# Kernel tuning notes

Hardware: AMD Instinct MI355X
Metric: run time of the kernel (lower is better)

## Reference

```python
import jax, jax.numpy as jnp
import numpy as np

D, H = 8, 1024        # data_dim, hidden_size
ENC, HOR = 96, 336    # encode window, prediction horizon


def _cell(x, h, c, wih, whh, b):
    # PyTorch LSTM gate order: i, f, g, o
    g = x @ wih.T + h @ whh.T + b
    i, f, gg, o = jnp.split(g, 4, axis=-1)
    c2 = jax.nn.sigmoid(f) * c + jax.nn.sigmoid(i) * jnp.tanh(gg)
    h2 = jax.nn.sigmoid(o) * jnp.tanh(c2)
    return h2, c2


def _run_layer(xs, wih, whh, b, h0, c0):
    # xs: [T, B, in] -> outputs [T, B, out], final (h, c)
    def step(carry, xt):
        h, c = carry
        h2, c2 = _cell(xt, h, c, wih, whh, b)
        return (h2, c2), h2
    (hT, cT), hs = jax.lax.scan(step, (h0, c0), xs)
    return hs, hT, cT


def setup_inputs() -> dict:
    key = jax.random.key(0)
    ks = jax.random.split(key, 10)
    s = 1.0 / np.sqrt(H)
    inputs = jax.random.normal(ks[0], (64, ENC + HOR, D), dtype=jnp.float32)
    # lstm (2 layers, hidden H)
    w_ih0 = jax.random.normal(ks[1], (4 * H, D), dtype=jnp.float32) * s
    w_hh0 = jax.random.normal(ks[2], (4 * H, H), dtype=jnp.float32) * s
    b0 = jax.random.normal(ks[3], (4 * H,), dtype=jnp.float32) * s
    w_ih1 = jax.random.normal(ks[4], (4 * H, H), dtype=jnp.float32) * s
    w_hh1 = jax.random.normal(ks[5], (4 * H, H), dtype=jnp.float32) * s
    b1 = jax.random.normal(ks[6], (4 * H,), dtype=jnp.float32) * s
    # lstm2 (1 layer, hidden D)
    w_ih2 = jax.random.normal(ks[7], (4 * D, H), dtype=jnp.float32) * s
    w_hh2 = jax.random.normal(ks[8], (4 * D, D), dtype=jnp.float32) * s
    b2 = jax.random.normal(ks[9], (4 * D,), dtype=jnp.float32) * s
    return {"inputs": inputs, "w_ih0": w_ih0, "w_hh0": w_hh0, "b0": b0,
            "w_ih1": w_ih1, "w_hh1": w_hh1, "b1": b1,
            "w_ih2": w_ih2, "w_hh2": w_hh2, "b2": b2}


def reference(inputs, w_ih0, w_hh0, b0, w_ih1, w_hh1, b1, w_ih2, w_hh2, b2):
    x = inputs[..., :D]
    enc, y = x[:, :ENC], x[:, ENC:]          # [B,96,D], [B,336,D]
    B = enc.shape[0]
    zH = jnp.zeros((B, H), dtype=enc.dtype)
    zD = jnp.zeros((B, D), dtype=enc.dtype)

    # ---- encode: stacked LSTM over 96 steps ----
    xs = enc.transpose(1, 0, 2)              # [T,B,D]
    h1s, ha, ca = _run_layer(xs, w_ih0, w_hh0, b0, zH, zH)
    h2s, hb, cb = _run_layer(h1s, w_ih1, w_hh1, b1, zH, zH)
    hds, hd, cd = _run_layer(h2s, w_ih2, w_hh2, b2, zD, zD)
    pred0 = hds[-1]                          # [B,D]

    def dec(carry, _):
        p, ha, ca, hb, cb, hd, cd = carry
        ha, ca = _cell(p, ha, ca, w_ih0, w_hh0, b0)
        hb, cb = _cell(ha, hb, cb, w_ih1, w_hh1, b1)
        hd, cd = _cell(hb, hd, cd, w_ih2, w_hh2, b2)
        return (hd, ha, ca, hb, cb, hd, cd), hd

    _, preds = jax.lax.scan(dec, (pred0, ha, ca, hb, cb, hd, cd), None,
                            length=HOR - 1)  # [335,B,D]
    pred = jnp.concatenate([pred0[None], preds], axis=0).transpose(1, 0, 2)  # [B,336,D]
    loss = jnp.mean((pred - y) ** 2, axis=(0, 1))  # [D]
    return pred, y, loss
```

## Files before the change

### kernel.cpp

```cpp
#include <hip/hip_runtime.h>
#include <math.h>

#define B64 64
#define H 1024
#define DD 8
#define ENC 96
#define HOR 336
#define TT 432
#define NSTEP 431
#define NBLK 256
#define KS0 32
#define KS1 64

typedef __attribute__((ext_vector_type(8))) short short8;
typedef __attribute__((ext_vector_type(4))) float f32x4;
typedef unsigned long long ull;

__device__ __forceinline__ unsigned short f2bf(float x) {
    union { float f; unsigned u; } v; v.f = x;
    unsigned r = v.u + 0x7fffu + ((v.u >> 16) & 1u);
    return (unsigned short)(r >> 16);
}
__device__ __forceinline__ float sigm(float x) {
    return __builtin_amdgcn_rcpf(1.0f + __expf(-x));
}
__device__ __forceinline__ float ftanh(float x) {
    float e = __expf(fminf(x, 10.0f) * 2.0f);
    return (e - 1.0f) * __builtin_amdgcn_rcpf(e + 1.0f);
}

__device__ __forceinline__ short8 cload(const unsigned short* p) {
    const ull* q = (const ull*)p;
    ull lo = __hip_atomic_load(q,     __ATOMIC_RELAXED, __HIP_MEMORY_SCOPE_AGENT);
    ull hi = __hip_atomic_load(q + 1, __ATOMIC_RELAXED, __HIP_MEMORY_SCOPE_AGENT);
    union { ull u[2]; short8 s; } v; v.u[0] = lo; v.u[1] = hi;
    return v.s;
}
__device__ __forceinline__ void cstore8(ull* p, ull v) {
    __hip_atomic_store(p, v, __ATOMIC_RELAXED, __HIP_MEMORY_SCOPE_AGENT);
}


__global__ void zero_k(unsigned int* __restrict__ p, int n) {
    for (int i = blockIdx.x * 256 + threadIdx.x; i < n; i += gridDim.x * 256) p[i] = 0u;
}

__global__ void pack0_k(const float* __restrict__ w, unsigned short* __restrict__ dst) {
    const int total = 128 * 2 * KS0 * 64 * 8;
    for (int idx = blockIdx.x * 256 + threadIdx.x; idx < total; idx += gridDim.x * 256) {
        int j = idx & 7, lane = (idx >> 3) & 63, ks = (idx >> 9) & 31, nt = (idx >> 14) & 1, nb = idx >> 15;
        int rr = nt * 16 + (lane & 15);
        int row = nb * 8 + (rr >> 2) + 1024 * (rr & 3);
        int k = ks * 32 + ((lane >> 4) << 3) + j;
        dst[idx] = f2bf(w[row * 1024 + k]);
    }
}

__global__ void pack1_k(const float* __restrict__ wih, const float* __restrict__ whh,
                        unsigned short* __restrict__ dst) {
    const int total = 128 * 2 * KS1 * 64 * 8;
    for (int idx = blockIdx.x * 256 + threadIdx.x; idx < total; idx += gridDim.x * 256) {
        int j = idx & 7, lane = (idx >> 3) & 63, ks = (idx >> 9) & 63, nt = (idx >> 15) & 1, nb = idx >> 16;
        int rr = nt * 16 + (lane & 15);
        int row = nb * 8 + (rr >> 2) + 1024 * (rr & 3);
        int k = ks * 32 + ((lane >> 4) << 3) + j;
        float v = (k < 1024) ? wih[row * 1024 + k] : whh[row * 1024 + (k - 1024)];
        dst[idx] = f2bf(v);
    }
}

__global__ void pack2_k(const float* __restrict__ w, unsigned short* __restrict__ dst) {
    const int total = 2 * KS0 * 64 * 8;
    for (int idx = blockIdx.x * 256 + threadIdx.x; idx < total; idx += gridDim.x * 256) {
        int j = idx & 7, lane = (idx >> 3) & 63, ks = (idx >> 9) & 31, nt = (idx >> 14) & 1;
        int rr = nt * 16 + (lane & 15);
        int row = (rr >> 2) + 8 * (rr & 3);
        int k = ks * 32 + ((lane >> 4) << 3) + j;
        dst[idx] = f2bf(w[row * 1024 + k]);
    }
}

__global__ void copy_y_k(const float* __restrict__ inp, float* __restrict__ y) {
    const int total = B64 * HOR * DD;
    for (int i = blockIdx.x * 256 + threadIdx.x; i < total; i += gridDim.x * 256) {
        int b = i / (HOR * DD);
        int rem = i - b * (HOR * DD);
        y[i] = inp[b * (TT * DD) + ENC * DD + rem];
    }
}

__global__ void loss_k(const float* __restrict__ pred, const float* __restrict__ y,
                       float* __restrict__ loss) {
    __shared__ float part[256];
    int tid = threadIdx.x;
    int dd = tid & 7, cc = tid >> 3;
    float s = 0.f;
    for (int i = cc; i < B64 * HOR; i += 32) {
        float d = pred[i * 8 + dd] - y[i * 8 + dd];
        s += d * d;
    }
    part[tid] = s;
    __syncthreads();
    if (tid < 8) {
        float t = 0.f;
        for (int r = 0; r < 32; ++r) t += part[r * 8 + tid];
        loss[tid] = t / (float)(B64 * HOR);
    }
}

__device__ __forceinline__ void gbar_arrive(unsigned* dom, int rb, unsigned ep) {
    if (threadIdx.x == 0) {
        __builtin_amdgcn_s_waitcnt(0x0f70);
        __hip_atomic_store(dom + rb * 32, ep, __ATOMIC_RELAXED,
                           __HIP_MEMORY_SCOPE_SYSTEM);
    }
}
__device__ __forceinline__ void gbar_wait(unsigned* dom, unsigned ep) {
    const int tid = threadIdx.x;
    if (tid < 64) {
        const unsigned* f0 = dom + tid * 32;
        const unsigned* f1 = dom + (tid + 64) * 32;
        for (;;) {
            unsigned a = __hip_atomic_load(f0, __ATOMIC_RELAXED, __HIP_MEMORY_SCOPE_SYSTEM);
            unsigned b = __hip_atomic_load(f1, __ATOMIC_RELAXED, __HIP_MEMORY_SCOPE_SYSTEM);
            if (__all((a >= ep) && (b >= ep))) break;
        }
    }
    __syncthreads();
}

__global__ __launch_bounds__(256, 1) void persist_k(
    const unsigned short* __restrict__ Wp0,
    const unsigned short* __restrict__ Wp1,
    const unsigned short* __restrict__ Wp2,
    const float* __restrict__ wih0, const float* __restrict__ b0v,
    const float* __restrict__ b1v,
    const float* __restrict__ whh2, const float* __restrict__ b2v,
    const float* __restrict__ inp,
    unsigned short* __restrict__ H0a, unsigned short* __restrict__ H0b,
    unsigned short* __restrict__ H1a, unsigned short* __restrict__ H1b,
    unsigned* __restrict__ bar0, float* __restrict__ pred)
{
    const int tid = threadIdx.x;
    const int wv = tid >> 6, lane = tid & 63;
    const int blk = blockIdx.x;
    const int bg = blk & 1, rb = blk >> 1;
    const int bl = tid & 31, u = tid >> 5;
    const int mtl = bl >> 4, m16 = bl & 15;
    unsigned* dom = bar0 + (bg << 13);

    __shared__ float red1[16 * 272];
    __shared__ float red2[16 * 272];
    __shared__ float h2x[32 * 9];
    __shared__ ull hstage[32][2];

    for (int i = tid; i < 32 * 9; i += 256) h2x[i] = 0.f;

    short8 Wr0[2][8], Wr1h0[2][8], Wr1h1[2][8];
    {
        const short8* p0 = (const short8*)Wp0;
        const short8* p1 = (const short8*)Wp1;
        #pragma unroll
        for (int ot = 0; ot < 2; ++ot)
            #pragma unroll
            for (int kk = 0; kk < 8; ++kk) {
                Wr0[ot][kk]   = p0[((rb * 2 + ot) * KS0 + 8 * wv + kk) * 64 + lane];
                Wr1h0[ot][kk] = p1[((rb * 2 + ot) * KS1 + 8 * wv + kk) * 64 + lane];
                Wr1h1[ot][kk] = p1[((rb * 2 + ot) * KS1 + 32 + 8 * wv + kk) * 64 + lane];
            }
    }
    float wih0r[4][8], whh2r[4][8], b0r[4], b1r[4], b2r[4];
    #pragma unroll
    for (int g = 0; g < 4; ++g) {
        int row = rb * 8 + u + 1024 * g;
        #pragma unroll
        for (int d = 0; d < 8; ++d) wih0r[g][d] = wih0[row * 8 + d];
        b0r[g] = b0v[row];
        b1r[g] = b1v[row];
        int row2 = u + 8 * g;
        #pragma unroll
        for (int d = 0; d < 8; ++d) whh2r[g][d] = whh2[row2 * 8 + d];
        b2r[g] = b2v[row2];
    }
    float c0r = 0.f, c1r = 0.f, c2r = 0.f;
    unsigned ep = 0;

    auto redWrite = [&](float* red, f32x4 (&acc)[2][2]) {
        #pragma unroll
        for (int m = 0; m < 2; ++m)
            #pragma unroll
            for (int ot = 0; ot < 2; ++ot) {
                int base = ((wv * 2 + m) * 2 + ot) * 272 + (lane & 15) * 17 + (lane >> 4) * 4;
                #pragma unroll
                for (int r = 0; r < 4; ++r) red[base + r] = acc[m][ot][r];
            }
    };
    auto redSum = [&](const float* red, int g) {
        int rr = u * 4 + g, ot = rr >> 4, rr16 = rr & 15;
        float s = 0.f;
        #pragma unroll
        for (int w2 = 0; w2 < 4; ++w2)
            s += red[((w2 * 2 + mtl) * 2 + ot) * 272 + rr16 * 17 + m16];
        return s;
    };
    auto hPublish = [&](unsigned short* Hw) {
        __syncthreads();
        if (tid < 32) {
            int b = bg * 32 + tid;
            int chunk = ((b >> 4) * KS0 + (rb >> 2)) * 64 + ((b & 15) | ((rb & 3) << 4));
            cstore8((ull*)Hw + chunk * 2,     hstage[tid][0]);
            cstore8((ull*)Hw + chunk * 2 + 1, hstage[tid][1]);
        }
    };

    short8 qa[8], qb[8];
    {
        union { ull u[2]; short8 s; } z; z.u[0] = 0; z.u[1] = 0;
        #pragma unroll
        for (int kk = 0; kk < 8; ++kk) { qa[kk] = z.s; qb[kk] = z.s; }
    }
    __syncthreads();

    {
        float xv[8];
        int b = bg * 32 + bl;
        #pragma unroll
        for (int d = 0; d < 8; ++d) xv[d] = inp[(b * TT + 0) * DD + d];
        float g4[4];
        #pragma unroll
        for (int g = 0; g < 4; ++g) {
            float s = b0r[g];
            #pragma unroll
            for (int d = 0; d < 8; ++d) s += wih0r[g][d] * xv[d];
            g4[g] = s;
        }
        c0r = sigm(g4[0]) * ftanh(g4[2]);
        float hn = sigm(g4[3]) * ftanh(c0r);
        ((unsigned short*)hstage)[bl * 8 + u] = f2bf(hn);
        hPublish(H0a);
    }
    gbar_arrive(dom, rb, ++ep);

    short8 pa[8], pb[8];

    for (int t = 0; t < NSTEP; ++t) {
        const int par = t & 1;
        const unsigned short* H0cur = par ? H0b : H0a;
        unsigned short* H1w = par ? H1b : H1a;
        unsigned short* H0nxt = par ? H0a : H0b;
        const bool last = (t == NSTEP - 1);

        f32x4 acc[2][2];
        #pragma unroll
        for (int m = 0; m < 2; ++m)
            #pragma unroll
            for (int ot = 0; ot < 2; ++ot) acc[m][ot] = (f32x4){0.f, 0.f, 0.f, 0.f};
        #pragma unroll
        for (int kk = 0; kk < 8; ++kk) {
            #pragma unroll
            for (int ot = 0; ot < 2; ++ot) {
                acc[0][ot] = __builtin_amdgcn_mfma_f32_16x16x32_bf16(qa[kk], Wr1h1[ot][kk], acc[0][ot], 0, 0, 0);
                acc[1][ot] = __builtin_amdgcn_mfma_f32_16x16x32_bf16(qb[kk], Wr1h1[ot][kk], acc[1][ot], 0, 0, 0);
            }
        }
        gbar_wait(dom, ep);

        {
            #pragma unroll
            for (int kk = 0; kk < 8; ++kk) {
                pa[kk] = cload(H0cur + (((bg * 2 + 0) * KS0 + 8 * wv + kk) * 64 + lane) * 8);
                pb[kk] = cload(H0cur + (((bg * 2 + 1) * KS0 + 8 * wv + kk) * 64 + lane) * 8);
            }
            #pragma unroll
            for (int kk = 0; kk < 8; ++kk) {
                #pragma unroll
                for (int ot = 0; ot < 2; ++ot) {
                    acc[0][ot] = __builtin_amdgcn_mfma_f32_16x16x32_bf16(pa[kk], Wr1h0[ot][kk], acc[0][ot], 0, 0, 0);
                    acc[1][ot] = __builtin_amdgcn_mfma_f32_16x16x32_bf16(pb[kk], Wr1h0[ot][kk], acc[1][ot], 0, 0, 0);
                }
            }
            redWrite(red1, acc);
            __syncthreads();
            float g4[4];
            #pragma unroll
            for (int g = 0; g < 4; ++g) g4[g] = b1r[g] + redSum(red1, g);
            c1r = sigm(g4[1]) * c1r + sigm(g4[0]) * ftanh(g4[2]);
            float hn = sigm(g4[3]) * ftanh(c1r);
            ((unsigned short*)hstage)[bl * 8 + u] = f2bf(hn);
            hPublish(H1w);
        }
        gbar_arrive(dom, rb, ++ep);

        if (!last) {
            f32x4 a1[2][2];
            #pragma unroll
            for (int m = 0; m < 2; ++m)
                #pragma unroll
                for (int ot = 0; ot < 2; ++ot) a1[m][ot] = (f32x4){0.f, 0.f, 0.f, 0.f};
            #pragma unroll
            for (int kk = 0; kk < 8; ++kk) {
                #pragma unroll
                for (int ot = 0; ot < 2; ++ot) {
                    a1[0][ot] = __builtin_amdgcn_mfma_f32_16x16x32_bf16(pa[kk], Wr0[ot][kk], a1[0][ot], 0, 0, 0);
                    a1[1][ot] = __builtin_amdgcn_mfma_f32_16x16x32_bf16(pb[kk], Wr0[ot][kk], a1[1][ot], 0, 0, 0);
                }
            }
            redWrite(red2, a1);
        }
        gbar_wait(dom, ep);

        {
            const short8* p2w = (const short8*)Wp2;
            short8 w2[2][8];
            #pragma unroll
            for (int ot = 0; ot < 2; ++ot)
                #pragma unroll
                for (int kk = 0; kk < 8; ++kk)
                    w2[ot][kk] = p2w[(ot * KS0 + 8 * wv + kk) * 64 + lane];
            #pragma unroll
            for (int kk = 0; kk < 8; ++kk) {
                qa[kk] = cload(H1w + (((bg * 2 + 0) * KS0 + 8 * wv + kk) * 64 + lane) * 8);
                qb[kk] = cload(H1w + (((bg * 2 + 1) * KS0 + 8 * wv + kk) * 64 + lane) * 8);
            }
            f32x4 a3[2][2];
            #pragma unroll
            for (int m = 0; m < 2; ++m)
                #pragma unroll
                for (int ot = 0; ot < 2; ++ot) a3[m][ot] = (f32x4){0.f, 0.f, 0.f, 0.f};
            #pragma unroll
            for (int kk = 0; kk < 8; ++kk) {
                #pragma unroll
                for (int ot = 0; ot < 2; ++ot) {
                    a3[0][ot] = __builtin_amdgcn_mfma_f32_16x16x32_bf16(qa[kk], w2[ot][kk], a3[0][ot], 0, 0, 0);
                    a3[1][ot] = __builtin_amdgcn_mfma_f32_16x16x32_bf16(qb[kk], w2[ot][kk], a3[1][ot], 0, 0, 0);
                }
            }
            redWrite(red1, a3);
            __syncthreads();
            float xo[8];
            #pragma unroll
            for (int d = 0; d < 8; ++d) xo[d] = h2x[bl * 9 + d];
            float g4[4];
            #pragma unroll
            for (int g = 0; g < 4; ++g) {
                float s = b2r[g] + redSum(red1, g);
                #pragma unroll
                for (int d = 0; d < 8; ++d) s += whh2r[g][d] * xo[d];
                g4[g] = s;
            }
            float cn = sigm(g4[1]) * c2r + sigm(g4[0]) * ftanh(g4[2]);
            c2r = cn;
            float hn2 = sigm(g4[3]) * ftanh(cn);
            __syncthreads();
            h2x[bl * 9 + u] = hn2;
            if (rb == 0 && t >= ENC - 1)
                pred[((bg * 32 + bl) * HOR + (t - (ENC - 1))) * DD + u] = hn2;

            if (!last) {
                __syncthreads();
                const int tt = t + 1;
                float xv[8];
                if (tt < ENC) {
                    int b = bg * 32 + bl;
                    #pragma unroll
                    for (int d = 0; d < 8; ++d) xv[d] = inp[(b * TT + tt) * DD + d];
                } else {
                    #pragma unroll
                    for (int d = 0; d < 8; ++d) xv[d] = h2x[bl * 9 + d];
                }
                float g1[4];
                #pragma unroll
                for (int g = 0; g < 4; ++g) {
                    float s = b0r[g] + redSum(red2, g);
                    #pragma unroll
                    for (int d = 0; d < 8; ++d) s += wih0r[g][d] * xv[d];
                    g1[g] = s;
                }
                c0r = sigm(g1[1]) * c0r + sigm(g1[0]) * ftanh(g1[2]);
                float hn0 = sigm(g1[3]) * ftanh(c0r);
                ((unsigned short*)hstage)[bl * 8 + u] = f2bf(hn0);
                hPublish(H0nxt);
                gbar_arrive(dom, rb, ++ep);
            }
        }
    }
}


extern "C" void kernel_launch(void* const* d_in, const int* in_sizes, int n_in,
                              void* d_out, int out_size, void* d_ws, size_t ws_size,
                              hipStream_t stream)
{
    const float* inp  = (const float*)d_in[0];
    const float* wih0 = (const float*)d_in[1];
    const float* whh0 = (const float*)d_in[2];
    const float* b0v  = (const float*)d_in[3];
    const float* wih1 = (const float*)d_in[4];
    const float* whh1 = (const float*)d_in[5];
    const float* b1v  = (const float*)d_in[6];
    const float* wih2 = (const float*)d_in[7];
    const float* whh2 = (const float*)d_in[8];
    const float* b2v  = (const float*)d_in[9];
    float* out = (float*)d_out;

    char* base = (char*)d_ws;
    size_t off = 0;
    auto carve = [&](size_t bytes) -> void* {
        void* p = base + off;
        off += (bytes + 255) & ~((size_t)255);
        return p;
    };
    unsigned short* Wp0 = (unsigned short*)carve((size_t)128 * 2 * KS0 * 64 * 8 * 2);
    unsigned short* Wp1 = (unsigned short*)carve((size_t)128 * 2 * KS1 * 64 * 8 * 2);
    unsigned short* Wp2 = (unsigned short*)carve((size_t)2 * KS0 * 64 * 8 * 2);
    size_t state_off = off;
    unsigned short* H0a = (unsigned short*)carve(B64 * H * 2);
    unsigned short* H0b = (unsigned short*)carve(B64 * H * 2);
    unsigned short* H1a = (unsigned short*)carve(B64 * H * 2);
    unsigned short* H1b = (unsigned short*)carve(B64 * H * 2);
    unsigned* bar = (unsigned*)carve(2 * 8192 * 4);
    size_t state_bytes = off - state_off;
    if (off > ws_size) return;

    zero_k<<<64, 256, 0, stream>>>((unsigned int*)(base + state_off), (int)(state_bytes / 4));
    pack0_k<<<2048, 256, 0, stream>>>(whh0, Wp0);
    pack1_k<<<4096, 256, 0, stream>>>(wih1, whh1, Wp1);
    pack2_k<<<32, 256, 0, stream>>>(wih2, Wp2);
    copy_y_k<<<672, 256, 0, stream>>>(inp, out + 172032);

    persist_k<<<NBLK, 256, 0, stream>>>(Wp0, Wp1, Wp2, wih0, b0v, b1v, whh2, b2v,
                                        inp, H0a, H0b, H1a, H1b, bar, out);

    loss_k<<<1, 256, 0, stream>>>(out, out + 172032, out + 344064);
}
```

Measured before the change: 3.569 ms.

## Hoist layer-2 weights to registers and publish layer-0 state before layer-2 during encode

Layer-2 weights (Wr2) are now loaded once into registers instead of being reloaded from global memory every step. During the encode phase, where the next layer-0 input does not depend on layer-2 output, the layer-0 state is computed, published and the barrier arrival signalled before the layer-2 cell runs, so other blocks can proceed sooner. In decode the layer-0 gate partial sums are prepared before the layer-2 cell. Prediction writes are spread across blocks instead of all coming from block 0. The cost is higher register pressure from the extra weight fragments, which could lower occupancy or cause spills.

```diff
diff --git a/kernel.cpp b/kernel.cpp
--- a/kernel.cpp
+++ b/kernel.cpp
@@ -156,10 +156,11 @@
 
     for (int i = tid; i < 32 * 9; i += 256) h2x[i] = 0.f;
 
-    short8 Wr0[2][8], Wr1h0[2][8], Wr1h1[2][8];
+    short8 Wr0[2][8], Wr1h0[2][8], Wr1h1[2][8], Wr2[2][8];
     {
         const short8* p0 = (const short8*)Wp0;
         const short8* p1 = (const short8*)Wp1;
+        const short8* p2 = (const short8*)Wp2;
         #pragma unroll
         for (int ot = 0; ot < 2; ++ot)
             #pragma unroll
@@ -167,6 +168,7 @@
                 Wr0[ot][kk]   = p0[((rb * 2 + ot) * KS0 + 8 * wv + kk) * 64 + lane];
                 Wr1h0[ot][kk] = p1[((rb * 2 + ot) * KS1 + 8 * wv + kk) * 64 + lane];
                 Wr1h1[ot][kk] = p1[((rb * 2 + ot) * KS1 + 32 + 8 * wv + kk) * 64 + lane];
+                Wr2[ot][kk]   = p2[(ot * KS0 + 8 * wv + kk) * 64 + lane];
             }
     }
     float wih0r[4][8], whh2r[4][8], b0r[4], b1r[4], b2r[4];
@@ -212,6 +214,41 @@
             cstore8((ull*)Hw + chunk * 2 + 1, hstage[tid][1]);
         }
     };
+    auto runP3 = [&](short8 (&qa)[8], short8 (&qb)[8], int t) {
+        f32x4 a3[2][2];
+        #pragma unroll
+        for (int m = 0; m < 2; ++m)
+            #pragma unroll
+            for (int ot = 0; ot < 2; ++ot) a3[m][ot] = (f32x4){0.f, 0.f, 0.f, 0.f};
+        #pragma unroll
+        for (int kk = 0; kk < 8; ++kk) {
+            #pragma unroll
+            for (int ot = 0; ot < 2; ++ot) {
+                a3[0][ot] = __builtin_amdgcn_mfma_f32_16x16x32_bf16(qa[kk], Wr2[ot][kk], a3[0][ot], 0, 0, 0);
+                a3[1][ot] = __builtin_amdgcn_mfma_f32_16x16x32_bf16(qb[kk], Wr2[ot][kk], a3[1][ot], 0, 0, 0);
+            }
+        }
+        redWrite(red1, a3);
+        __syncthreads();
+        float xo[8];
+        #pragma unroll
+        for (int d = 0; d < 8; ++d) xo[d] = h2x[bl * 9 + d];
+        float g4[4];
+        #pragma unroll
+        for (int g = 0; g < 4; ++g) {
+            float s = b2r[g] + redSum(red1, g);
+            #pragma unroll
+            for (int d = 0; d < 8; ++d) s += whh2r[g][d] * xo[d];
+            g4[g] = s;
+        }
+        float cn = sigm(g4[1]) * c2r + sigm(g4[0]) * ftanh(g4[2]);
+        c2r = cn;
+        float hn2 = sigm(g4[3]) * ftanh(cn);
+        __syncthreads();
+        h2x[bl * 9 + u] = hn2;
+        if (t >= ENC - 1 && ((((bl << 3) | u) >> 1) == rb))
+            pred[((bg * 32 + bl) * HOR + (t - (ENC - 1))) * DD + u] = hn2;
+    };
 
     short8 qa[8], qb[8];
     {
@@ -310,70 +347,20 @@
         gbar_wait(dom, ep);
 
         {
-            const short8* p2w = (const short8*)Wp2;
-            short8 w2[2][8];
-            #pragma unroll
-            for (int ot = 0; ot < 2; ++ot)
-                #pragma unroll
-                for (int kk = 0; kk < 8; ++kk)
-                    w2[ot][kk] = p2w[(ot * KS0 + 8 * wv + kk) * 64 + lane];
             #pragma unroll
             for (int kk = 0; kk < 8; ++kk) {
                 qa[kk] = cload(H1w + (((bg * 2 + 0) * KS0 + 8 * wv + kk) * 64 + lane) * 8);
                 qb[kk] = cload(H1w + (((bg * 2 + 1) * KS0 + 8 * wv + kk) * 64 + lane) * 8);
             }
-            f32x4 a3[2][2];
-            #pragma unroll
-            for (int m = 0; m < 2; ++m)
-                #pragma unroll
-                for (int ot = 0; ot < 2; ++ot) a3[m][ot] = (f32x4){0.f, 0.f, 0.f, 0.f};
-            #pragma unroll
-            for (int kk = 0; kk < 8; ++kk) {
-                #pragma unroll
-                for (int ot = 0; ot < 2; ++ot) {
-                    a3[0][ot] = __builtin_amdgcn_mfma_f32_16x16x32_bf16(qa[kk], w2[ot][kk], a3[0][ot], 0, 0, 0);
-                    a3[1][ot] = __builtin_amdgcn_mfma_f32_16x16x32_bf16(qb[kk], w2[ot][kk], a3[1][ot], 0, 0, 0);
-                }
-            }
-            redWrite(red1, a3);
-            __syncthreads();
-            float xo[8];
-            #pragma unroll
-            for (int d = 0; d < 8; ++d) xo[d] = h2x[bl * 9 + d];
-            float g4[4];
-            #pragma unroll
-            for (int g = 0; g < 4; ++g) {
-                float s = b2r[g] + redSum(red1, g);
-                #pragma unroll
-                for (int d = 0; d < 8; ++d) s += whh2r[g][d] * xo[d];
-                g4[g] = s;
-            }
-            float cn = sigm(g4[1]) * c2r + sigm(g4[0]) * ftanh(g4[2]);
-            c2r = cn;
-            float hn2 = sigm(g4[3]) * ftanh(cn);
-            __syncthreads();
-            h2x[bl * 9 + u] = hn2;
-            if (rb == 0 && t >= ENC - 1)
-                pred[((bg * 32 + bl) * HOR + (t - (ENC - 1))) * DD + u] = hn2;
-
-            if (!last) {
-                __syncthreads();
-                const int tt = t + 1;
-                float xv[8];
-                if (tt < ENC) {
-                    int b = bg * 32 + bl;
-                    #pragma unroll
-                    for (int d = 0; d < 8; ++d) xv[d] = inp[(b * TT + tt) * DD + d];
-                } else {
-                    #pragma unroll
-                    for (int d = 0; d < 8; ++d) xv[d] = h2x[bl * 9 + d];
-                }
+            const int tt = t + 1;
+            if (!last && tt < ENC) {
                 float g1[4];
+                int b = bg * 32 + bl;
                 #pragma unroll
                 for (int g = 0; g < 4; ++g) {
                     float s = b0r[g] + redSum(red2, g);
                     #pragma unroll
-                    for (int d = 0; d < 8; ++d) s += wih0r[g][d] * xv[d];
+                    for (int d = 0; d < 8; ++d) s += wih0r[g][d] * inp[(b * TT + tt) * DD + d];
                     g1[g] = s;
                 }
                 c0r = sigm(g1[1]) * c0r + sigm(g1[0]) * ftanh(g1[2]);
@@ -381,6 +368,33 @@
                 ((unsigned short*)hstage)[bl * 8 + u] = f2bf(hn0);
                 hPublish(H0nxt);
                 gbar_arrive(dom, rb, ++ep);
+                runP3(qa, qb, t);
+            } else {
+                float g1p[4];
+                if (!last) {
+                    #pragma unroll
+                    for (int g = 0; g < 4; ++g) g1p[g] = b0r[g] + redSum(red2, g);
+                }
+                runP3(qa, qb, t);
+                if (!last) {
+                    __syncthreads();
+                    float xv[8];
+                    #pragma unroll
+                    for (int d = 0; d < 8; ++d) xv[d] = h2x[bl * 9 + d];
+                    float g1[4];
+                    #pragma unroll
+                    for (int g = 0; g < 4; ++g) {
+                        float s = g1p[g];
+                        #pragma unroll
+                        for (int d = 0; d < 8; ++d) s += wih0r[g][d] * xv[d];
+                        g1[g] = s;
+                    }
+                    c0r = sigm(g1[1]) * c0r + sigm(g1[0]) * ftanh(g1[2]);
+                    float hn0 = sigm(g1[3]) * ftanh(c0r);
+                    ((unsigned short*)hstage)[bl * 8 + u] = f2bf(hn0);
+                    hPublish(H0nxt);
+                    gbar_arrive(dom, rb, ++ep);
+                }
             }
         }
     }
```

After: 3.574 ms. About the same (+0.1%).
